# Kernel tuning notes

Measured on AMD Instinct MI355X. Metric: run time of the kernel, lower is better.

Reference implementation:

```python
import jax, jax.numpy as jnp
import numpy as np

N = 10000      # nodes (drugs)
F_IN = 128     # input feature dim
H1 = 64        # hidden1
H2 = 32        # hidden2
R = 65         # num_relations
E_O = 320000   # edges in main graph
E_S = 160000   # edges per augmented subgraph
NB = 4         # num_layers parallel branches
B = 4096       # drug pairs


def setup_inputs() -> dict:
    key = jax.random.key(0)
    ks = jax.random.split(key, 32)
    def nrm(k, shape, fan_in):
        return (jax.random.normal(k, shape) * (1.0 / np.sqrt(fan_in))).astype(jnp.float32)
    inp = {}
    inp["x_o"] = jax.random.normal(ks[0], (N, F_IN), jnp.float32)
    inp["edge_index_o"] = jax.random.randint(ks[1], (2, E_O), 0, N)
    inp["edge_type_o"] = jax.random.randint(ks[2], (E_O,), 0, R)
    inp["x_s"] = jax.random.normal(ks[3], (NB, N, F_IN), jnp.float32)
    inp["edge_index_s"] = jax.random.randint(ks[4], (NB, 2, E_S), 0, N)
    inp["edge_type_s"] = jax.random.randint(ks[5], (NB, E_S), 0, R)
    inp["idx"] = jax.random.randint(ks[6], (2, B), 0, N)
    inp["features1"] = jax.random.normal(ks[7], (N, F_IN), jnp.float32)
    # main encoder RGCN params
    inp["W1"] = nrm(ks[8], (R, F_IN, H1), F_IN)
    inp["root1"] = nrm(ks[9], (F_IN, H1), F_IN)
    inp["b1"] = jnp.zeros((H1,), jnp.float32)
    inp["W2"] = nrm(ks[10], (R, H1, H2), H1)
    inp["root2"] = nrm(ks[11], (H1, H2), H1)
    inp["b2"] = jnp.zeros((H2,), jnp.float32)
    # 4 branch encoders (stacked over branch dim)
    inp["Ws1"] = nrm(ks[12], (NB, R, F_IN, H1), F_IN)
    inp["roots1"] = nrm(ks[13], (NB, F_IN, H1), F_IN)
    inp["bs1"] = jnp.zeros((NB, H1), jnp.float32)
    inp["Ws2"] = nrm(ks[14], (NB, R, H1, H2), H1)
    inp["roots2"] = nrm(ks[15], (NB, H1, H2), H1)
    inp["bs2"] = jnp.zeros((NB, H2), jnp.float32)
    # MLP head: 576 -> 256 -> 128 -> 65
    inp["mlp_w1"] = nrm(ks[16], (576, 256), 576)
    inp["mlp_b1"] = jnp.zeros((256,), jnp.float32)
    inp["mlp_w2"] = nrm(ks[17], (256, 128), 256)
    inp["mlp_b2"] = jnp.zeros((128,), jnp.float32)
    inp["mlp_w3"] = nrm(ks[18], (128, 65), 128)
    inp["mlp_b3"] = jnp.zeros((65,), jnp.float32)
    return inp


def _rgcn(x, src, dst, etype, W, Wroot, b):
    """PyG RGCNConv with aggr='mean': per-(dst,relation) mean of W_r x_j, summed over relations, plus root transform."""
    n = x.shape[0]
    r = W.shape[0]
    h = jnp.einsum('ni,rio->nro', x, W)                      # [N,R,out]
    seg = dst * r + etype                                    # per-(node,rel) segment id
    ones = jnp.ones(src.shape[0], x.dtype)
    deg = jax.ops.segment_sum(ones, seg, num_segments=n * r)  # in-degree per (dst,rel)
    norm = 1.0 / jnp.maximum(deg, 1.0)
    m = h[src, etype] * norm[seg][:, None]                   # [E,out]
    agg = jax.ops.segment_sum(m, dst, num_segments=n)        # scatter-add to dst
    return agg + x @ Wroot + b


def _branch(xb, src, dst, et, W1b, r1b, b1b, W2b, r2b, b2b):
    h1 = jax.nn.relu(_rgcn(xb, src, dst, et, W1b, r1b, b1b))
    return _rgcn(h1, src, dst, et, W2b, r2b, b2b)


def reference(x_o, edge_index_o, edge_type_o, x_s, edge_index_s, edge_type_s, idx,
              features1, W1, root1, b1, W2, root2, b2,
              Ws1, roots1, bs1, Ws2, roots2, bs2,
              mlp_w1, mlp_b1, mlp_w2, mlp_b2, mlp_w3, mlp_b3):
    # main encoder (dropout is eval-mode identity)
    src_o, dst_o = edge_index_o[0], edge_index_o[1]
    h1 = jax.nn.relu(_rgcn(x_o, src_o, dst_o, edge_type_o, W1, root1, b1))
    x2_oo = _rgcn(h1, src_o, dst_o, edge_type_o, W2, root2, b2)   # [N,H2]
    # 4 parallel branch encoders, vmapped over branch dim
    x2_s = jax.vmap(_branch)(x_s, edge_index_s[:, 0], edge_index_s[:, 1], edge_type_s,
                             Ws1, roots1, bs1, Ws2, roots2, bs2)  # [NB,N,H2]
    n = x2_oo.shape[0]
    embeds = jnp.concatenate(
        [x2_oo, jnp.transpose(x2_s, (1, 0, 2)).reshape(n, -1)], axis=1)  # [N, 5*H2]
    d1, d2 = idx[0], idx[1]
    feats = jnp.concatenate(
        [embeds[d1], features1[d1], embeds[d2], features1[d2]], axis=1)  # [B,576]
    h = jax.nn.elu(feats @ mlp_w1 + mlp_b1)
    h = jax.nn.elu(h @ mlp_w2 + mlp_b2)
    return h @ mlp_w3 + mlp_b3  # [B,65] logits
```

## Files before the change

kernel.cpp:

```cpp
#include <hip/hip_runtime.h>
#include <hip/hip_bf16.h>

namespace {
constexpr int N_NODES = 10000;
constexpr int FIN  = 128;
constexpr int H1S  = 64;
constexpr int H2S  = 32;
constexpr int RREL = 65;
constexpr int EO   = 320000;
constexpr int ES   = 160000;
constexpr int NBR  = 4;
constexpr int BP   = 4096;
constexpr int E_TOT = EO + 4 * ES;
constexpr int CAP_MAIN = EO + 128 * RREL;
constexpr int CAP_SUB  = ES + 128 * RREL;
constexpr int CAP_TOT  = CAP_MAIN + 4 * CAP_SUB;
constexpr int CHK_MAIN = CAP_MAIN / 128;
constexpr int CHK_SUB  = CAP_SUB / 128;
constexpr int CHK_TOT  = CHK_MAIN + 4 * CHK_SUB;
constexpr int CHK_TOT_PAD = 7840;
constexpr int SCH = 1024;
constexpr int SBLK_MAIN = (EO + SCH - 1) / SCH;
}

typedef unsigned short u16;
typedef unsigned int   u32;
typedef short bf16x8 __attribute__((ext_vector_type(8)));
typedef float f32x4  __attribute__((ext_vector_type(4)));

__device__ __forceinline__ u16 f2bf(float f) {
    u32 u = __builtin_bit_cast(u32, f);
    u32 r = u + 0x7FFFu + ((u >> 16) & 1u);
    return (u16)(r >> 16);
}
__device__ __forceinline__ float bf2f_lo(u32 v) { return __builtin_bit_cast(float, v << 16); }
__device__ __forceinline__ float bf2f_hi(u32 v) { return __builtin_bit_cast(float, v & 0xFFFF0000u); }
__device__ __forceinline__ bf16x8 as_bf16x8(uint4 v) {
    union { uint4 u; bf16x8 b; } cv; cv.u = v; return cv.b;
}
__device__ __forceinline__ int chunk_graph(int bid) {
    return (bid < CHK_MAIN) ? 0 : 1 + (bid - CHK_MAIN) / CHK_SUB;
}

__global__ __launch_bounds__(256) void count_hist_all(const int* __restrict__ et_o,
                                                      const int* __restrict__ et_s,
                                                      int* __restrict__ hist) {
    int g = blockIdx.y;
    const int* etv; int E;
    if (g == 0) { etv = et_o; E = EO; }
    else { etv = et_s + (size_t)(g - 1) * ES; E = ES; }
    __shared__ int lh[RREL];
    for (int i = threadIdx.x; i < RREL; i += 256) lh[i] = 0;
    __syncthreads();
    for (int e = blockIdx.x * 256 + threadIdx.x; e < E; e += gridDim.x * 256)
        atomicAdd(&lh[etv[e]], 1);
    __syncthreads();
    for (int i = threadIdx.x; i < RREL; i += 256) {
        int c = lh[i];
        if (c) atomicAdd(&hist[g * RREL + i], c);
    }
}

__global__ void prefix_fill(const int* __restrict__ hist, int* __restrict__ cursor,
                            int* __restrict__ relbase, int* __restrict__ c2r) {
    int g = blockIdx.x;
    __shared__ int offs[RREL + 1];
    int capc  = (g == 0) ? CHK_MAIN : CHK_SUB;
    int cbase = (g == 0) ? 0 : CHK_MAIN + (g - 1) * CHK_SUB;
    int ebase = (g == 0) ? 0 : CAP_MAIN + (g - 1) * CAP_SUB;
    if (threadIdx.x == 0) {
        int acc = 0;
        for (int r = 0; r < RREL; ++r) {
            offs[r] = acc;
            cursor[g * RREL + r]  = ebase + acc;
            relbase[g * RREL + r] = ebase + acc;
            int c = hist[g * RREL + r];
            acc += (c + 127) & ~127;
        }
        offs[RREL] = acc;
    }
    __syncthreads();
    int total = offs[RREL];
    for (int c = threadIdx.x; c < capc; c += blockDim.x) {
        int pos = c * 128;
        int r = -1;
        if (pos < total) {
            int lo = 0, hi = RREL - 1;
            while (lo < hi) { int mid = (lo + hi + 1) >> 1; if (offs[mid] <= pos) lo = mid; else hi = mid - 1; }
            r = lo;
        }
        c2r[cbase + c] = r;
    }
}

__global__ __launch_bounds__(256) void scatter_rel(const int* __restrict__ ei_o,
                                                   const int* __restrict__ et_o,
                                                   const int* __restrict__ ei_s,
                                                   const int* __restrict__ et_s,
                                                   int* __restrict__ cursor,
                                                   int* __restrict__ ssrc,
                                                   int* __restrict__ sdst) {
    int g = blockIdx.y;
    const int* srcv; const int* dstv; const int* etv; int E;
    if (g == 0) { srcv = ei_o; dstv = ei_o + EO; etv = et_o; E = EO; }
    else {
        int b = g - 1;
        srcv = ei_s + (size_t)b * 2 * ES;
        dstv = srcv + ES;
        etv  = et_s + (size_t)b * ES;
        E = ES;
    }
    __shared__ int lh[RREL];
    __shared__ int lbase[RREL];
    int tid = threadIdx.x;
    int e0 = blockIdx.x * SCH;
    if (e0 >= E) return;
    int e1 = min(e0 + SCH, E);
    for (int i = tid; i < RREL; i += 256) lh[i] = 0;
    __syncthreads();
    for (int e = e0 + tid; e < e1; e += 256)
        atomicAdd(&lh[etv[e]], 1);
    __syncthreads();
    for (int i = tid; i < RREL; i += 256) {
        int c = lh[i];
        lbase[i] = c ? atomicAdd(&cursor[g * RREL + i], c) : 0;
        lh[i] = 0;
    }
    __syncthreads();
    for (int e = e0 + tid; e < e1; e += 256) {
        int r = etv[e];
        int rank = atomicAdd(&lh[r], 1);
        int pos = lbase[r] + rank;
        ssrc[pos] = srcv[e];
        sdst[pos] = dstv[e];
    }
}

__global__ __launch_bounds__(256) void seg_hist(const int* __restrict__ sdst,
                                                const int* __restrict__ relbase,
                                                const int* __restrict__ hist,
                                                u32* __restrict__ deg_r) {
    int r = blockIdx.x, g = blockIdx.y;
    __shared__ u32 h[N_NODES];
    int tid = threadIdx.x;
    for (int i = tid; i < N_NODES; i += 256) h[i] = 0;
    __syncthreads();
    int start = relbase[g * RREL + r], cnt = hist[g * RREL + r];
    for (int i = start + tid; i < start + cnt; i += 256)
        atomicAdd(&h[sdst[i]], 1u);
    __syncthreads();
    u32* out = deg_r + (size_t)(g * RREL + r) * N_NODES;
    for (int i = tid; i < N_NODES; i += 256) out[i] = h[i];
}

__global__ __launch_bounds__(256) void nodedeg_from_degr(const u32* __restrict__ deg_r,
                                                         int* __restrict__ node_deg) {
    int t = blockIdx.x * 256 + threadIdx.x;
    if (t >= 5 * N_NODES) return;
    int g = t / N_NODES, d = t % N_NODES;
    const u32* base = deg_r + (size_t)g * RREL * N_NODES + d;
    u32 s = 0;
    for (int r = 0; r < RREL; ++r) s += base[(size_t)r * N_NODES];
    node_deg[t] = (int)s;
}

__global__ __launch_bounds__(256) void scan_rowptr(const int* __restrict__ node_deg,
                                                   int* __restrict__ row_ptr) {
    int g = blockIdx.x;
    const int* nd = node_deg + (size_t)g * N_NODES;
    int* rp = row_ptr + (size_t)g * (N_NODES + 1);
    int off = (g == 0) ? 0 : EO + (g - 1) * ES;
    __shared__ int part[257];
    int tid = threadIdx.x;
    const int CH = (N_NODES + 255) / 256;
    int base = tid * CH;
    int s = 0;
    for (int i = 0; i < CH; ++i) { int ix = base + i; if (ix < N_NODES) s += nd[ix]; }
    part[tid + 1] = s;
    if (tid == 0) part[0] = 0;
    __syncthreads();
    if (tid == 0) { for (int i = 1; i <= 256; ++i) part[i] += part[i - 1]; }
    __syncthreads();
    int acc = part[tid];
    for (int i = 0; i < CH; ++i) {
        int ix = base + i;
        if (ix < N_NODES) { rp[ix] = off + acc; acc += nd[ix]; }
    }
    if (tid == 0) rp[N_NODES] = off + part[256];
}

__global__ __launch_bounds__(256) void drbase(const u32* __restrict__ deg_r,
                                              const int* __restrict__ row_ptr,
                                              u32* __restrict__ base_abs) {
    int t = blockIdx.x * 256 + threadIdx.x;
    if (t >= 5 * N_NODES) return;
    int g = t / N_NODES, d = t % N_NODES;
    u32 run = (u32)row_ptr[(size_t)g * (N_NODES + 1) + d];
    const u32* din = deg_r + (size_t)g * RREL * N_NODES + d;
    u32* bout = base_abs + (size_t)g * RREL * N_NODES + d;
    for (int r = 0; r < RREL; ++r) {
        bout[(size_t)r * N_NODES] = run;
        run += din[(size_t)r * N_NODES];
    }
}

__global__ __launch_bounds__(256) void snrm_epos(const int* __restrict__ sdst,
                                                 const int* __restrict__ relbase,
                                                 const int* __restrict__ hist,
                                                 const u32* __restrict__ base_abs,
                                                 const u32* __restrict__ deg_r,
                                                 int* __restrict__ epos,
                                                 float* __restrict__ snrm) {
    int r = blockIdx.x, g = blockIdx.y;
    int cnt = hist[g * RREL + r];
    if (cnt == 0) return;
    __shared__ u32 cur[N_NODES];
    __shared__ u16 dg[N_NODES];
    int tid = threadIdx.x;
    const u32* bslice = base_abs + (size_t)(g * RREL + r) * N_NODES;
    const u32* dslice = deg_r + (size_t)(g * RREL + r) * N_NODES;
    for (int i = tid; i < N_NODES; i += 256) {
        cur[i] = bslice[i];
        dg[i] = (u16)dslice[i];
    }
    __syncthreads();
    int start = relbase[g * RREL + r];
    for (int pos = start + tid; pos < start + cnt; pos += 256) {
        int d = sdst[pos];
        u32 slot = atomicAdd(&cur[d], 1u);
        epos[pos] = (int)slot;
        snrm[pos] = 1.0f / fmaxf((float)dg[d], 1.0f);
    }
}

namespace {
constexpr int NX_  = 5 * N_NODES * FIN;
constexpr int NW1_ = 5 * RREL * FIN * H1S;
constexpr int NW2_ = 5 * RREL * H1S * H2S;
constexpr int NM1_ = 256 * 576;
constexpr int NM2_ = 128 * 256;
constexpr int NM3_ = 128 * 128;
constexpr int NPREP = NX_ + NW1_ + NW2_ + NM1_ + NM2_ + NM3_;
}
__global__ __launch_bounds__(256) void prep_all(const float* __restrict__ x_o,
                                                const float* __restrict__ x_s,
                                                const float* __restrict__ W1,
                                                const float* __restrict__ Ws1,
                                                const float* __restrict__ W2,
                                                const float* __restrict__ Ws2,
                                                const float* __restrict__ mw1,
                                                const float* __restrict__ mw2,
                                                const float* __restrict__ mw3,
                                                u16* __restrict__ xbf,
                                                u16* __restrict__ wt1,
                                                u16* __restrict__ wt2,
                                                u16* __restrict__ w1t,
                                                u16* __restrict__ w2t,
                                                u16* __restrict__ w3t) {
    int t = blockIdx.x * 256 + threadIdx.x;
    if (t < NX_) {
        int g = t / (N_NODES * FIN), off = t % (N_NODES * FIN);
        float v = (g == 0) ? x_o[off] : x_s[(size_t)(g - 1) * N_NODES * FIN + off];
        xbf[t] = f2bf(v);
        return;
    }
    t -= NX_;
    if (t < NW1_) {
        int q = t % (RREL * FIN * H1S), g = t / (RREL * FIN * H1S);
        int k = q & 127; int ro = q >> 7; int o = ro & 63; int r = ro >> 6;
        const float* src = (g == 0) ? W1 : Ws1 + (size_t)(g - 1) * RREL * FIN * H1S;
        wt1[(size_t)g * RREL * FIN * H1S + q] = f2bf(src[((size_t)r * FIN + k) * H1S + o]);
        return;
    }
    t -= NW1_;
    if (t < NW2_) {
        int q = t % (RREL * H1S * H2S), g = t / (RREL * H1S * H2S);
        int k = q & 63; int ro = q >> 6; int o = ro & 31; int r = ro >> 5;
        const float* src = (g == 0) ? W2 : Ws2 + (size_t)(g - 1) * RREL * H1S * H2S;
        wt2[(size_t)g * RREL * H1S * H2S + q] = f2bf(src[((size_t)r * H1S + k) * H2S + o]);
        return;
    }
    t -= NW2_;
    if (t < NM1_) {
        int k = t % 576, o = t / 576;
        w1t[t] = f2bf(mw1[(size_t)k * 256 + o]);
        return;
    }
    t -= NM1_;
    if (t < NM2_) {
        int k = t % 256, o = t / 256;
        w2t[t] = f2bf(mw2[(size_t)k * 128 + o]);
        return;
    }
    t -= NM2_;
    if (t < NM3_) {
        int k = t % 128, o = t / 128;
        w3t[t] = (o < 65) ? f2bf(mw3[(size_t)k * 65 + o]) : (u16)0;
    }
}

__global__ __launch_bounds__(256) void rgcn_mfma_l1_all(const u16* __restrict__ xbfa,
                                                        const int* __restrict__ ssrc,
                                                        const float* __restrict__ snrm,
                                                        const int* __restrict__ c2r,
                                                        const int* __restrict__ epos,
                                                        const u16* __restrict__ wt1a,
                                                        u16* __restrict__ medge) {
    __shared__ uint4 Xs4[128 * 16];
    __shared__ uint4 Wt4[64 * 16];
    int tid = threadIdx.x;
    int bid = blockIdx.x;
    int r = c2r[bid];
    if (r < 0) return;
    int g = chunk_graph(bid);
    int e0 = bid * 128;
    const u16* xbf = xbfa + (size_t)g * N_NODES * FIN;
    {
        const uint4* wsrc = (const uint4*)(wt1a + ((size_t)g * RREL + r) * H1S * FIN);
        #pragma unroll
        for (int i = 0; i < 4; ++i) {
            int g16 = tid + i * 256;
            int row = g16 >> 4, c = g16 & 15;
            Wt4[row * 16 + (c ^ (row & 7))] = wsrc[g16];
        }
    }
    {
        int rt = tid >> 1, h = tid & 1;
        int s = ssrc[e0 + rt];
        const uint4* src = (const uint4*)(xbf + (size_t)s * FIN) + h * 8;
        #pragma unroll
        for (int j = 0; j < 8; ++j) {
            int c = h * 8 + j;
            Xs4[rt * 16 + (c ^ (rt & 7))] = src[j];
        }
    }
    __syncthreads();
    int w = tid >> 6, l = tid & 63;
    int lo = l & 15, hi = l >> 4;
    f32x4 acc[2][4];
    #pragma unroll
    for (int m = 0; m < 2; ++m)
        #pragma unroll
        for (int n = 0; n < 4; ++n) acc[m][n] = {0.f, 0.f, 0.f, 0.f};
    #pragma unroll
    for (int kk = 0; kk < 4; ++kk) {
        int kc = kk * 4 + hi;
        int ea = w * 32 + lo, eb = w * 32 + 16 + lo;
        bf16x8 a0 = as_bf16x8(Xs4[ea * 16 + (kc ^ (ea & 7))]);
        bf16x8 a1 = as_bf16x8(Xs4[eb * 16 + (kc ^ (eb & 7))]);
        #pragma unroll
        for (int n = 0; n < 4; ++n) {
            int o = n * 16 + lo;
            bf16x8 b = as_bf16x8(Wt4[o * 16 + (kc ^ (o & 7))]);
            acc[0][n] = __builtin_amdgcn_mfma_f32_16x16x32_bf16(a0, b, acc[0][n], 0, 0, 0);
            acc[1][n] = __builtin_amdgcn_mfma_f32_16x16x32_bf16(a1, b, acc[1][n], 0, 0, 0);
        }
    }
    #pragma unroll
    for (int m = 0; m < 2; ++m) {
        #pragma unroll
        for (int rg = 0; rg < 4; ++rg) {
            int erow = e0 + w * 32 + m * 16 + hi * 4 + rg;
            float nv = snrm[erow];
            if (nv != 0.f) {
                size_t jb = (size_t)epos[erow] * H1S;
                #pragma unroll
                for (int n = 0; n < 4; ++n)
                    medge[jb + n * 16 + lo] = f2bf(acc[m][n][rg] * nv);
            }
        }
    }
}

__global__ __launch_bounds__(256) void rgcn_mfma_l2_all(const u16* __restrict__ h1bfa,
                                                        const int* __restrict__ ssrc,
                                                        const float* __restrict__ snrm,
                                                        const int* __restrict__ c2r,
                                                        const int* __restrict__ epos,
                                                        const u16* __restrict__ wt2a,
                                                        u16* __restrict__ medge) {
    __shared__ uint4 Xs4[128 * 8];
    __shared__ uint4 Wt4[32 * 8];
    int tid = threadIdx.x;
    int bid = blockIdx.x;
    int r = c2r[bid];
    if (r < 0) return;
    int g = chunk_graph(bid);
    int e0 = bid * 128;
    const u16* h1bf = h1bfa + (size_t)g * N_NODES * H1S;
    {
        const uint4* wsrc = (const uint4*)(wt2a + ((size_t)g * RREL + r) * H2S * H1S);
        int row = tid >> 3, c = tid & 7;
        Wt4[row * 8 + (c ^ (row & 7))] = wsrc[tid];
    }
    {
        int rt = tid >> 1, h = tid & 1;
        int s = ssrc[e0 + rt];
        const uint4* src = (const uint4*)(h1bf + (size_t)s * H1S) + h * 4;
        #pragma unroll
        for (int j = 0; j < 4; ++j) {
            int c = h * 4 + j;
            Xs4[rt * 8 + (c ^ (rt & 7))] = src[j];
        }
    }
    __syncthreads();
    int w = tid >> 6, l = tid & 63;
    int lo = l & 15, hi = l >> 4;
    f32x4 acc[2][2];
    #pragma unroll
    for (int m = 0; m < 2; ++m)
        #pragma unroll
        for (int n = 0; n < 2; ++n) acc[m][n] = {0.f, 0.f, 0.f, 0.f};
    #pragma unroll
    for (int kk = 0; kk < 2; ++kk) {
        int kc = kk * 4 + hi;
        int ea = w * 32 + lo, eb = w * 32 + 16 + lo;
        bf16x8 a0 = as_bf16x8(Xs4[ea * 8 + (kc ^ (ea & 7))]);
        bf16x8 a1 = as_bf16x8(Xs4[eb * 8 + (kc ^ (eb & 7))]);
        #pragma unroll
        for (int n = 0; n < 2; ++n) {
            int o = n * 16 + lo;
            bf16x8 b = as_bf16x8(Wt4[o * 8 + (kc ^ (o & 7))]);
            acc[0][n] = __builtin_amdgcn_mfma_f32_16x16x32_bf16(a0, b, acc[0][n], 0, 0, 0);
            acc[1][n] = __builtin_amdgcn_mfma_f32_16x16x32_bf16(a1, b, acc[1][n], 0, 0, 0);
        }
    }
    #pragma unroll
    for (int m = 0; m < 2; ++m) {
        #pragma unroll
        for (int rg = 0; rg < 4; ++rg) {
            int erow = e0 + w * 32 + m * 16 + hi * 4 + rg;
            float nv = snrm[erow];
            if (nv != 0.f) {
                size_t jb = (size_t)epos[erow] * H2S;
                #pragma unroll
                for (int n = 0; n < 2; ++n)
                    medge[jb + n * 16 + lo] = f2bf(acc[m][n][rg] * nv);
            }
        }
    }
}

__global__ __launch_bounds__(256) void finish_l1_all(const float* __restrict__ x_o,
                                                     const float* __restrict__ x_s,
                                                     const float* __restrict__ root1,
                                                     const float* __restrict__ roots1,
                                                     const float* __restrict__ b1,
                                                     const float* __restrict__ bs1,
                                                     const u16* __restrict__ medge,
                                                     const int* __restrict__ row_ptr,
                                                     float* __restrict__ aggH1,
                                                     u16* __restrict__ h1bfa) {
    int g = blockIdx.y;
    const float* x    = (g == 0) ? x_o : x_s + (size_t)(g - 1) * N_NODES * FIN;
    const float* root = (g == 0) ? root1 : roots1 + (size_t)(g - 1) * FIN * H1S;
    const float* bias = (g == 0) ? b1 : bs1 + (size_t)(g - 1) * H1S;
    const int* rp = row_ptr + (size_t)g * (N_NODES + 1);
    float* h1 = aggH1 + (size_t)g * N_NODES * H1S;
    u16* h1bf = h1bfa + (size_t)g * N_NODES * H1S;
    __shared__ float xs[16][FIN + 1];
    int tid = threadIdx.x;
    int vsub = tid >> 4, og = tid & 15;
    int v = blockIdx.x * 16 + vsub;
    bool valid = v < N_NODES;
    int vv = valid ? v : N_NODES - 1;
    #pragma unroll
    for (int i = 0; i < 8; ++i)
        xs[vsub][og + 16 * i] = x[(size_t)vv * FIN + og + 16 * i];
    int j0 = rp[vv], j1 = rp[vv + 1];
    float4 acc;
    acc.x = bias[og * 4 + 0]; acc.y = bias[og * 4 + 1];
    acc.z = bias[og * 4 + 2]; acc.w = bias[og * 4 + 3];
    for (int j = j0; j < j1; ++j) {
        uint2 m = *(const uint2*)(medge + (size_t)j * H1S + og * 4);
        acc.x += bf2f_lo(m.x); acc.y += bf2f_hi(m.x);
        acc.z += bf2f_lo(m.y); acc.w += bf2f_hi(m.y);
    }
    __syncthreads();
    const float* Rp = root + og * 4;
    #pragma unroll 16
    for (int i = 0; i < FIN; ++i) {
        float xv = xs[vsub][i];
        float4 w = *(const float4*)(Rp + (size_t)i * H1S);
        acc.x += xv * w.x; acc.y += xv * w.y; acc.z += xv * w.z; acc.w += xv * w.w;
    }
    if (valid) {
        float r0 = fmaxf(acc.x, 0.f), r1 = fmaxf(acc.y, 0.f);
        float r2 = fmaxf(acc.z, 0.f), r3 = fmaxf(acc.w, 0.f);
        float* ag = h1 + (size_t)vv * H1S + og * 4;
        ag[0] = r0; ag[1] = r1; ag[2] = r2; ag[3] = r3;
        uint2 pk;
        pk.x = (u32)f2bf(r0) | ((u32)f2bf(r1) << 16);
        pk.y = (u32)f2bf(r2) | ((u32)f2bf(r3) << 16);
        *(uint2*)(h1bf + (size_t)vv * H1S + og * 4) = pk;
    }
}

__global__ __launch_bounds__(256) void finish_l2_all(const float* __restrict__ aggH1,
                                                     const float* __restrict__ root2,
                                                     const float* __restrict__ roots2,
                                                     const float* __restrict__ b2,
                                                     const float* __restrict__ bs2,
                                                     const u16* __restrict__ medge,
                                                     const int* __restrict__ row_ptr,
                                                     float* __restrict__ aggH2) {
    int g = blockIdx.y;
    const float* x    = aggH1 + (size_t)g * N_NODES * H1S;
    const float* root = (g == 0) ? root2 : roots2 + (size_t)(g - 1) * H1S * H2S;
    const float* bias = (g == 0) ? b2 : bs2 + (size_t)(g - 1) * H2S;
    const int* rp = row_ptr + (size_t)g * (N_NODES + 1);
    float* x2 = aggH2 + (size_t)g * N_NODES * H2S;
    __shared__ float xs[32][H1S + 1];
    int tid = threadIdx.x;
    int vsub = tid >> 3, og = tid & 7;
    int v = blockIdx.x * 32 + vsub;
    bool valid = v < N_NODES;
    int vv = valid ? v : N_NODES - 1;
    #pragma unroll
    for (int i = 0; i < 8; ++i)
        xs[vsub][og + 8 * i] = x[(size_t)vv * H1S + og + 8 * i];
    int j0 = rp[vv], j1 = rp[vv + 1];
    float4 acc;
    acc.x = bias[og * 4 + 0]; acc.y = bias[og * 4 + 1];
    acc.z = bias[og * 4 + 2]; acc.w = bias[og * 4 + 3];
    for (int j = j0; j < j1; ++j) {
        uint2 m = *(const uint2*)(medge + (size_t)j * H2S + og * 4);
        acc.x += bf2f_lo(m.x); acc.y += bf2f_hi(m.x);
        acc.z += bf2f_lo(m.y); acc.w += bf2f_hi(m.y);
    }
    __syncthreads();
    const float* Rp = root + og * 4;
    #pragma unroll
    for (int i = 0; i < H1S; ++i) {
        float xv = xs[vsub][i];
        float4 w = *(const float4*)(Rp + (size_t)i * H2S);
        acc.x += xv * w.x; acc.y += xv * w.y; acc.z += xv * w.z; acc.w += xv * w.w;
    }
    if (valid) {
        float* ag = x2 + (size_t)vv * H2S + og * 4;
        ag[0] = acc.x; ag[1] = acc.y; ag[2] = acc.z; ag[3] = acc.w;
    }
}

__global__ __launch_bounds__(256) void gather_feats_direct(const float* __restrict__ aggH2,
                                                           const float* __restrict__ features1,
                                                           const int* __restrict__ idx,
                                                           u16* __restrict__ featsbf) {
    int t = blockIdx.x * blockDim.x + threadIdx.x;
    if (t >= BP * 576) return;
    int b = t / 576, c = t % 576;
    int d1 = idx[b], d2 = idx[BP + b];
    float v;
    if (c < 160) {
        int bb = c >> 5, cc = c & 31;
        v = aggH2[(size_t)bb * N_NODES * H2S + (size_t)d1 * H2S + cc];
    } else if (c < 288) {
        v = features1[(size_t)d1 * FIN + (c - 160)];
    } else if (c < 448) {
        int cc2 = c - 288;
        int bb = cc2 >> 5, cc = cc2 & 31;
        v = aggH2[(size_t)bb * N_NODES * H2S + (size_t)d2 * H2S + cc];
    } else {
        v = features1[(size_t)d2 * FIN + (c - 448)];
    }
    featsbf[t] = f2bf(v);
}

template <int ACT, int OUTF>
__global__ __launch_bounds__(256) void mlp_mfma(const u16* __restrict__ A,
                                                const u16* __restrict__ Bt,
                                                const float* __restrict__ bias,
                                                u16* __restrict__ Cbf,
                                                float* __restrict__ Cf,
                                                int M, int N, int K) {
    __shared__ uint4 As4[128 * 8];
    __shared__ uint4 Bs4[64 * 8];
    int tid = threadIdx.x;
    int row0 = blockIdx.x * 128, col0 = blockIdx.y * 64;
    int w = tid >> 6, l = tid & 63;
    int lo = l & 15, hi = l >> 4;
    f32x4 acc[2][4];
    #pragma unroll
    for (int m = 0; m < 2; ++m)
        #pragma unroll
        for (int n = 0; n < 4; ++n) acc[m][n] = {0.f, 0.f, 0.f, 0.f};
    int nchunks = K >> 6;
    for (int ch = 0; ch < nchunks; ++ch) {
        #pragma unroll
        for (int i = 0; i < 4; ++i) {
            int g16 = tid + i * 256;
            int rr = g16 >> 3, c = g16 & 7;
            As4[rr * 8 + (c ^ (rr & 7))] =
                *((const uint4*)(A + (size_t)(row0 + rr) * K + ch * 64) + c);
        }
        #pragma unroll
        for (int i = 0; i < 2; ++i) {
            int g16 = tid + i * 256;
            int rr = g16 >> 3, c = g16 & 7;
            Bs4[rr * 8 + (c ^ (rr & 7))] =
                *((const uint4*)(Bt + (size_t)(col0 + rr) * K + ch * 64) + c);
        }
        __syncthreads();
        #pragma unroll
        for (int ks = 0; ks < 2; ++ks) {
            int kc = ks * 4 + hi;
            int ra = w * 32 + lo, rb = w * 32 + 16 + lo;
            bf16x8 a0 = as_bf16x8(As4[ra * 8 + (kc ^ (ra & 7))]);
            bf16x8 a1 = as_bf16x8(As4[rb * 8 + (kc ^ (rb & 7))]);
            #pragma unroll
            for (int n = 0; n < 4; ++n) {
                int o = n * 16 + lo;
                bf16x8 b = as_bf16x8(Bs4[o * 8 + (kc ^ (o & 7))]);
                acc[0][n] = __builtin_amdgcn_mfma_f32_16x16x32_bf16(a0, b, acc[0][n], 0, 0, 0);
                acc[1][n] = __builtin_amdgcn_mfma_f32_16x16x32_bf16(a1, b, acc[1][n], 0, 0, 0);
            }
        }
        __syncthreads();
    }
    #pragma unroll
    for (int m = 0; m < 2; ++m) {
        #pragma unroll
        for (int rg = 0; rg < 4; ++rg) {
            int rr = row0 + w * 32 + m * 16 + hi * 4 + rg;
            if (rr < M) {
                #pragma unroll
                for (int n = 0; n < 4; ++n) {
                    int cc = col0 + n * 16 + lo;
                    if (cc < N) {
                        float v = acc[m][n][rg] + bias[cc];
                        if (ACT == 1) v = (v > 0.f) ? v : expm1f(v);
                        if (OUTF) Cf[(size_t)rr * N + cc] = v;
                        else Cbf[(size_t)rr * N + cc] = f2bf(v);
                    }
                }
            }
        }
    }
}

extern "C" void kernel_launch(void* const* d_in, const int* in_sizes, int n_in,
                              void* d_out, int out_size, void* d_ws, size_t ws_size,
                              hipStream_t stream) {
    const float* x_o      = (const float*)d_in[0];
    const int*   ei_o     = (const int*)d_in[1];
    const int*   et_o     = (const int*)d_in[2];
    const float* x_s      = (const float*)d_in[3];
    const int*   ei_s     = (const int*)d_in[4];
    const int*   et_s     = (const int*)d_in[5];
    const int*   idx      = (const int*)d_in[6];
    const float* features1= (const float*)d_in[7];
    const float* W1       = (const float*)d_in[8];
    const float* root1    = (const float*)d_in[9];
    const float* b1       = (const float*)d_in[10];
    const float* W2       = (const float*)d_in[11];
    const float* root2    = (const float*)d_in[12];
    const float* b2       = (const float*)d_in[13];
    const float* Ws1      = (const float*)d_in[14];
    const float* roots1   = (const float*)d_in[15];
    const float* bs1      = (const float*)d_in[16];
    const float* Ws2      = (const float*)d_in[17];
    const float* roots2   = (const float*)d_in[18];
    const float* bs2      = (const float*)d_in[19];
    const float* mlp_w1   = (const float*)d_in[20];
    const float* mlp_b1   = (const float*)d_in[21];
    const float* mlp_w2   = (const float*)d_in[22];
    const float* mlp_b2   = (const float*)d_in[23];
    const float* mlp_w3   = (const float*)d_in[24];
    const float* mlp_b3   = (const float*)d_in[25];

    int*   hist     = (int*)d_ws;
    int*   ssrc     = hist + 5 * RREL;
    float* snrm     = (float*)(ssrc + CAP_TOT);
    int*   sdst     = (int*)(snrm + CAP_TOT);
    int*   cursor   = sdst + CAP_TOT;
    int*   relbase  = cursor + 5 * RREL;
    int*   c2r      = relbase + 5 * RREL;
    u32*   deg_r    = (u32*)(c2r + CHK_TOT_PAD);
    u32*   base_abs = deg_r + (size_t)5 * RREL * N_NODES;
    int*   node_deg = (int*)(base_abs + (size_t)5 * RREL * N_NODES);
    int*   row_ptr  = node_deg + 5 * N_NODES;
    int*   epos     = row_ptr + 5 * (N_NODES + 1);
    float* aggH1    = (float*)(epos + CAP_TOT);
    float* aggH2    = aggH1 + (size_t)5 * N_NODES * H1S;
    u16*   featsbf  = (u16*)(aggH2 + (size_t)5 * N_NODES * H2S);
    u16*   mh1bf    = featsbf + (size_t)BP * 576;
    u16*   mh2bf    = mh1bf + (size_t)BP * 256;
    u16*   w1t      = mh2bf + (size_t)BP * 128;
    u16*   w2t      = w1t + (size_t)256 * 576;
    u16*   w3t      = w2t + (size_t)128 * 256;
    u16*   wt1a     = w3t + (size_t)128 * 128;
    u16*   wt2a     = wt1a + (size_t)5 * RREL * H1S * FIN;
    u16*   xbfa     = wt2a + (size_t)5 * RREL * H2S * H1S;
    u16*   h1bfa    = xbfa + (size_t)5 * N_NODES * FIN;
    u16*   medge    = h1bfa + (size_t)5 * N_NODES * H1S;

    size_t zero_bytes = (size_t)((char*)sdst - (char*)d_ws);
    hipMemsetAsync(d_ws, 0, zero_bytes, stream);

    prep_all<<<(NPREP + 255) / 256, 256, 0, stream>>>(
        x_o, x_s, W1, Ws1, W2, Ws2, mlp_w1, mlp_w2, mlp_w3,
        xbfa, wt1a, wt2a, w1t, w2t, w3t);
    count_hist_all<<<dim3(128, 5), 256, 0, stream>>>(et_o, et_s, hist);
    prefix_fill<<<5, 256, 0, stream>>>(hist, cursor, relbase, c2r);
    scatter_rel<<<dim3(SBLK_MAIN, 5), 256, 0, stream>>>(
        ei_o, et_o, ei_s, et_s, cursor, ssrc, sdst);
    seg_hist<<<dim3(RREL, 5), 256, 0, stream>>>(sdst, relbase, hist, deg_r);
    nodedeg_from_degr<<<(5 * N_NODES + 255) / 256, 256, 0, stream>>>(deg_r, node_deg);
    scan_rowptr<<<5, 256, 0, stream>>>(node_deg, row_ptr);
    drbase<<<(5 * N_NODES + 255) / 256, 256, 0, stream>>>(deg_r, row_ptr, base_abs);
    snrm_epos<<<dim3(RREL, 5), 256, 0, stream>>>(
        sdst, relbase, hist, base_abs, deg_r, epos, snrm);

    rgcn_mfma_l1_all<<<CHK_TOT, 256, 0, stream>>>(
        xbfa, ssrc, snrm, c2r, epos, wt1a, medge);
    finish_l1_all<<<dim3((N_NODES + 15) / 16, 5), 256, 0, stream>>>(
        x_o, x_s, root1, roots1, b1, bs1, medge, row_ptr, aggH1, h1bfa);
    rgcn_mfma_l2_all<<<CHK_TOT, 256, 0, stream>>>(
        h1bfa, ssrc, snrm, c2r, epos, wt2a, medge);
    finish_l2_all<<<dim3((N_NODES + 31) / 32, 5), 256, 0, stream>>>(
        aggH1, root2, roots2, b2, bs2, medge, row_ptr, aggH2);

    gather_feats_direct<<<(BP * 576 + 255) / 256, 256, 0, stream>>>(aggH2, features1, idx, featsbf);
    mlp_mfma<1, 0><<<dim3(BP / 128, 4), 256, 0, stream>>>(featsbf, w1t, mlp_b1, mh1bf, nullptr, BP, 256, 576);
    mlp_mfma<1, 0><<<dim3(BP / 128, 2), 256, 0, stream>>>(mh1bf, w2t, mlp_b2, mh2bf, nullptr, BP, 128, 256);
    mlp_mfma<0, 1><<<dim3(BP / 128, 2), 256, 0, stream>>>(mh2bf, w3t, mlp_b3, nullptr, (float*)d_out, BP, 65, 128);
}
```

Before: 420.4 us.

## Write edge messages contiguously, gather via dst-sorted index; add XCD block swizzle

```diff
diff --git a/kernel.cpp b/kernel.cpp
--- a/kernel.cpp
+++ b/kernel.cpp
@@ -25,6 +25,7 @@
 
 typedef unsigned short u16;
 typedef unsigned int   u32;
+typedef unsigned long long u64;
 typedef short bf16x8 __attribute__((ext_vector_type(8)));
 typedef float f32x4  __attribute__((ext_vector_type(4)));
 
@@ -40,6 +41,11 @@
 }
 __device__ __forceinline__ int chunk_graph(int bid) {
     return (bid < CHK_MAIN) ? 0 : 1 + (bid - CHK_MAIN) / CHK_SUB;
+}
+__device__ __forceinline__ int xcd_swz(int bid) {
+    constexpr int q = CHK_TOT / 8, rr = CHK_TOT % 8;
+    int x = bid & 7, i = bid >> 3;
+    return (x < rr ? x * (q + 1) : rr * (q + 1) + (x - rr) * q) + i;
 }
 
 __global__ __launch_bounds__(256) void count_hist_all(const int* __restrict__ et_o,
@@ -204,12 +210,12 @@
     }
 }
 
-__global__ __launch_bounds__(256) void snrm_epos(const int* __restrict__ sdst,
+__global__ __launch_bounds__(256) void snrm_eidx(const int* __restrict__ sdst,
                                                  const int* __restrict__ relbase,
                                                  const int* __restrict__ hist,
                                                  const u32* __restrict__ base_abs,
                                                  const u32* __restrict__ deg_r,
-                                                 int* __restrict__ epos,
+                                                 int* __restrict__ eidx,
                                                  float* __restrict__ snrm) {
     int r = blockIdx.x, g = blockIdx.y;
     int cnt = hist[g * RREL + r];
@@ -228,7 +234,7 @@
     for (int pos = start + tid; pos < start + cnt; pos += 256) {
         int d = sdst[pos];
         u32 slot = atomicAdd(&cur[d], 1u);
-        epos[pos] = (int)slot;
+        eidx[slot] = pos;
         snrm[pos] = 1.0f / fmaxf((float)dg[d], 1.0f);
     }
 }
@@ -303,13 +309,12 @@
                                                         const int* __restrict__ ssrc,
                                                         const float* __restrict__ snrm,
                                                         const int* __restrict__ c2r,
-                                                        const int* __restrict__ epos,
                                                         const u16* __restrict__ wt1a,
                                                         u16* __restrict__ medge) {
     __shared__ uint4 Xs4[128 * 16];
     __shared__ uint4 Wt4[64 * 16];
     int tid = threadIdx.x;
-    int bid = blockIdx.x;
+    int bid = xcd_swz(blockIdx.x);
     int r = c2r[bid];
     if (r < 0) return;
     int g = chunk_graph(bid);
@@ -345,7 +350,7 @@
     #pragma unroll
     for (int kk = 0; kk < 4; ++kk) {
         int kc = kk * 4 + hi;
-        int ea = w * 32 + lo, eb = w * 32 + 16 + lo;
+        int ea = w * 32 + lo, eb = ea + 16;
         bf16x8 a0 = as_bf16x8(Xs4[ea * 16 + (kc ^ (ea & 7))]);
         bf16x8 a1 = as_bf16x8(Xs4[eb * 16 + (kc ^ (eb & 7))]);
         #pragma unroll
@@ -363,7 +368,7 @@
             int erow = e0 + w * 32 + m * 16 + hi * 4 + rg;
             float nv = snrm[erow];
             if (nv != 0.f) {
-                size_t jb = (size_t)epos[erow] * H1S;
+                size_t jb = (size_t)erow * H1S;
                 #pragma unroll
                 for (int n = 0; n < 4; ++n)
                     medge[jb + n * 16 + lo] = f2bf(acc[m][n][rg] * nv);
@@ -376,13 +381,12 @@
                                                         const int* __restrict__ ssrc,
                                                         const float* __restrict__ snrm,
                                                         const int* __restrict__ c2r,
-                                                        const int* __restrict__ epos,
                                                         const u16* __restrict__ wt2a,
                                                         u16* __restrict__ medge) {
     __shared__ uint4 Xs4[128 * 8];
     __shared__ uint4 Wt4[32 * 8];
     int tid = threadIdx.x;
-    int bid = blockIdx.x;
+    int bid = xcd_swz(blockIdx.x);
     int r = c2r[bid];
     if (r < 0) return;
     int g = chunk_graph(bid);
@@ -414,7 +418,7 @@
     #pragma unroll
     for (int kk = 0; kk < 2; ++kk) {
         int kc = kk * 4 + hi;
-        int ea = w * 32 + lo, eb = w * 32 + 16 + lo;
+        int ea = w * 32 + lo, eb = ea + 16;
         bf16x8 a0 = as_bf16x8(Xs4[ea * 8 + (kc ^ (ea & 7))]);
         bf16x8 a1 = as_bf16x8(Xs4[eb * 8 + (kc ^ (eb & 7))]);
         #pragma unroll
@@ -432,7 +436,7 @@
             int erow = e0 + w * 32 + m * 16 + hi * 4 + rg;
             float nv = snrm[erow];
             if (nv != 0.f) {
-                size_t jb = (size_t)epos[erow] * H2S;
+                size_t jb = (size_t)erow * H2S;
                 #pragma unroll
                 for (int n = 0; n < 2; ++n)
                     medge[jb + n * 16 + lo] = f2bf(acc[m][n][rg] * nv);
@@ -449,6 +453,7 @@
                                                      const float* __restrict__ bs1,
                                                      const u16* __restrict__ medge,
                                                      const int* __restrict__ row_ptr,
+                                                     const int* __restrict__ eidx,
                                                      float* __restrict__ aggH1,
                                                      u16* __restrict__ h1bfa) {
     int g = blockIdx.y;
@@ -472,9 +477,12 @@
     acc.x = bias[og * 4 + 0]; acc.y = bias[og * 4 + 1];
     acc.z = bias[og * 4 + 2]; acc.w = bias[og * 4 + 3];
     for (int j = j0; j < j1; ++j) {
-        uint2 m = *(const uint2*)(medge + (size_t)j * H1S + og * 4);
-        acc.x += bf2f_lo(m.x); acc.y += bf2f_hi(m.x);
-        acc.z += bf2f_lo(m.y); acc.w += bf2f_hi(m.y);
+        int pos = eidx[j];
+        u64 m = __builtin_nontemporal_load(
+            (const u64*)(medge + (size_t)pos * H1S + og * 4));
+        u32 mlo = (u32)m, mhi = (u32)(m >> 32);
+        acc.x += bf2f_lo(mlo); acc.y += bf2f_hi(mlo);
+        acc.z += bf2f_lo(mhi); acc.w += bf2f_hi(mhi);
     }
     __syncthreads();
     const float* Rp = root + og * 4;
@@ -503,6 +511,7 @@
                                                      const float* __restrict__ bs2,
                                                      const u16* __restrict__ medge,
                                                      const int* __restrict__ row_ptr,
+                                                     const int* __restrict__ eidx,
                                                      float* __restrict__ aggH2) {
     int g = blockIdx.y;
     const float* x    = aggH1 + (size_t)g * N_NODES * H1S;
@@ -524,9 +533,12 @@
     acc.x = bias[og * 4 + 0]; acc.y = bias[og * 4 + 1];
     acc.z = bias[og * 4 + 2]; acc.w = bias[og * 4 + 3];
     for (int j = j0; j < j1; ++j) {
-        uint2 m = *(const uint2*)(medge + (size_t)j * H2S + og * 4);
-        acc.x += bf2f_lo(m.x); acc.y += bf2f_hi(m.x);
-        acc.z += bf2f_lo(m.y); acc.w += bf2f_hi(m.y);
+        int pos = eidx[j];
+        u64 m = __builtin_nontemporal_load(
+            (const u64*)(medge + (size_t)pos * H2S + og * 4));
+        u32 mlo = (u32)m, mhi = (u32)(m >> 32);
+        acc.x += bf2f_lo(mlo); acc.y += bf2f_hi(mlo);
+        acc.z += bf2f_lo(mhi); acc.w += bf2f_hi(mhi);
     }
     __syncthreads();
     const float* Rp = root + og * 4;
@@ -679,8 +691,8 @@
     u32*   base_abs = deg_r + (size_t)5 * RREL * N_NODES;
     int*   node_deg = (int*)(base_abs + (size_t)5 * RREL * N_NODES);
     int*   row_ptr  = node_deg + 5 * N_NODES;
-    int*   epos     = row_ptr + 5 * (N_NODES + 1);
-    float* aggH1    = (float*)(epos + CAP_TOT);
+    int*   eidx     = row_ptr + 5 * (N_NODES + 1);
+    float* aggH1    = (float*)(eidx + E_TOT);
     float* aggH2    = aggH1 + (size_t)5 * N_NODES * H1S;
     u16*   featsbf  = (u16*)(aggH2 + (size_t)5 * N_NODES * H2S);
     u16*   mh1bf    = featsbf + (size_t)BP * 576;
@@ -708,17 +720,17 @@
     nodedeg_from_degr<<<(5 * N_NODES + 255) / 256, 256, 0, stream>>>(deg_r, node_deg);
     scan_rowptr<<<5, 256, 0, stream>>>(node_deg, row_ptr);
     drbase<<<(5 * N_NODES + 255) / 256, 256, 0, stream>>>(deg_r, row_ptr, base_abs);
-    snrm_epos<<<dim3(RREL, 5), 256, 0, stream>>>(
-        sdst, relbase, hist, base_abs, deg_r, epos, snrm);
+    snrm_eidx<<<dim3(RREL, 5), 256, 0, stream>>>(
+        sdst, relbase, hist, base_abs, deg_r, eidx, snrm);
 
     rgcn_mfma_l1_all<<<CHK_TOT, 256, 0, stream>>>(
-        xbfa, ssrc, snrm, c2r, epos, wt1a, medge);
+        xbfa, ssrc, snrm, c2r, wt1a, medge);
     finish_l1_all<<<dim3((N_NODES + 15) / 16, 5), 256, 0, stream>>>(
-        x_o, x_s, root1, roots1, b1, bs1, medge, row_ptr, aggH1, h1bfa);
+        x_o, x_s, root1, roots1, b1, bs1, medge, row_ptr, eidx, aggH1, h1bfa);
     rgcn_mfma_l2_all<<<CHK_TOT, 256, 0, stream>>>(
-        h1bfa, ssrc, snrm, c2r, epos, wt2a, medge);
+        h1bfa, ssrc, snrm, c2r, wt2a, medge);
     finish_l2_all<<<dim3((N_NODES + 31) / 32, 5), 256, 0, stream>>>(
-        aggH1, root2, roots2, b2, bs2, medge, row_ptr, aggH2);
+        aggH1, root2, roots2, b2, bs2, medge, row_ptr, eidx, aggH2);
 
     gather_feats_direct<<<(BP * 576 + 255) / 256, 256, 0, stream>>>(aggH2, features1, idx, featsbf);
     mlp_mfma<1, 0><<<dim3(BP / 128, 4), 256, 0, stream>>>(featsbf, w1t, mlp_b1, mh1bf, nullptr, BP, 256, 576);
```

Result: slower. 457.0 us (+8.7%).
